# Kernel optimization log

Hardware: AMD Instinct MI355X
Metric: run time of the kernel (lower is better)

## Reference

```python
import jax, jax.numpy as jnp
import numpy as np

N, HIDDEN, HEADS, HEAD = 20000, 128, 8, 16
LAP, NBUCKETS, NBINS, MAXDEG, E = 16, 1024, 32, 64, 320000


def _mlp(x, W1, b1, W2, b2):
    return jax.nn.relu(x @ W1 + b1) @ W2 + b2


def _build_pairs(bq, bk, edge_index):
    """Host-side: P_LSH = {(i,j)!=: bq[i]==bk[j]} union graph edges, deduped.
    Mirrors _lsh_pairs + torch.unique (data-dependent size -> numpy)."""
    bq = np.asarray(bq); bk = np.asarray(bk); ei = np.asarray(edge_index)
    srcs = [ei[0].astype(np.int64)]; dsts = [ei[1].astype(np.int64)]
    common = np.intersect1d(np.unique(bq), np.unique(bk))
    for b in common:
        qn = np.nonzero(bq == b)[0]
        kn = np.nonzero(bk == b)[0]
        ii = np.repeat(qn, kn.size)
        jj = np.tile(kn, qn.size)
        m = ii != jj
        srcs.append(ii[m].astype(np.int64)); dsts.append(jj[m].astype(np.int64))
    src = np.concatenate(srcs); dst = np.concatenate(dsts)
    code = np.unique(src * np.int64(N) + dst)  # dedup pairs
    return jnp.asarray(code // N, jnp.int32), jnp.asarray(code % N, jnp.int32)


def setup_inputs() -> dict:
    key = jax.random.key(0)
    ks = jax.random.split(key, 16)
    rn = lambda k, sh, s=1.0: (jax.random.normal(k, sh, jnp.float32) * s)
    d_in = HIDDEN + LAP
    return {
        "Q": rn(ks[0], (N, HIDDEN)),
        "K": rn(ks[1], (N, HIDDEN)),
        "V": rn(ks[2], (N, HIDDEN)),
        "lap_pe": jax.random.uniform(ks[3], (N, LAP), jnp.float32),
        "W_q1": rn(ks[4], (d_in, HIDDEN), d_in ** -0.5), "b_q1": jnp.zeros((HIDDEN,), jnp.float32),
        "W_q2": rn(ks[5], (HIDDEN, NBUCKETS), HIDDEN ** -0.5), "b_q2": jnp.zeros((NBUCKETS,), jnp.float32),
        "W_k1": rn(ks[6], (d_in, HIDDEN), d_in ** -0.5), "b_k1": jnp.zeros((HIDDEN,), jnp.float32),
        "W_k2": rn(ks[7], (HIDDEN, NBUCKETS), HIDDEN ** -0.5), "b_k2": jnp.zeros((NBUCKETS,), jnp.float32),
        "spd_bias": rn(ks[8], (NBINS + 1, HEADS), 0.02),
        "deg_src_emb": rn(ks[9], (MAXDEG + 2, HEADS), 0.02),
        "deg_dst_emb": rn(ks[10], (MAXDEG + 2, HEADS), 0.02),
        "W_out": rn(ks[11], (HIDDEN, HIDDEN), HIDDEN ** -0.5), "b_out": jnp.zeros((HIDDEN,), jnp.float32),
        "spd_boundaries": jnp.linspace(0.0, 2.0, NBINS).astype(jnp.float32),
        "edge_index": jax.random.randint(ks[12], (2, E), 0, N, jnp.int32),
        "deg": jax.random.randint(ks[13], (N,), 0, MAXDEG + 1, jnp.int32),
    }


def reference(Q, K, V, lap_pe, W_q1, b_q1, W_q2, b_q2, W_k1, b_k1, W_k2, b_k2,
              spd_bias, deg_src_emb, deg_dst_emb, W_out, b_out, spd_boundaries,
              edge_index, deg):
    q_in = jnp.concatenate([Q, lap_pe], axis=-1)
    k_in = jnp.concatenate([K, lap_pe], axis=-1)
    l_q = _mlp(q_in, W_q1, b_q1, W_q2, b_q2)  # (N, B)
    l_k = _mlp(k_in, W_k1, b_k1, W_k2, b_k2)
    src, dst = _build_pairs(jnp.argmax(l_q, -1), jnp.argmax(l_k, -1), edge_index)

    Qh = Q.reshape(N, HEADS, HEAD)
    Kh = K.reshape(N, HEADS, HEAD)
    Vh = V.reshape(N, HEADS, HEAD)

    scores = jnp.einsum("ehd,ehd->eh", Qh[src], Kh[dst]) / (HEAD ** 0.5)  # (P, H)
    pe_dist = jnp.linalg.norm(lap_pe[src] - lap_pe[dst], axis=-1)
    spd_idx = jnp.searchsorted(spd_boundaries, pe_dist, side="left")  # torch.bucketize(right=False)
    scores = scores + spd_bias[spd_idx]
    dsrc = jnp.clip(deg[src], 0, MAXDEG + 1)
    ddst = jnp.clip(deg[dst], 0, MAXDEG + 1)
    scores = scores + deg_src_emb[dsrc] + deg_dst_emb[ddst]

    # pyg_softmax: segment softmax over src index
    m = jax.ops.segment_max(scores, src, num_segments=N)  # (N, H)
    m = jnp.where(jnp.isneginf(m), 0.0, m)
    ex = jnp.exp(scores - m[src])
    denom = jax.ops.segment_sum(ex, src, num_segments=N)
    alpha = ex / (denom[src] + 1e-16)  # dropout p=0 (eval)

    h = jax.ops.segment_sum(alpha[..., None] * Vh[dst], src, num_segments=N)
    h_global = h.reshape(N, HIDDEN) @ W_out + b_out
    return h_global, l_q, l_k
```

## Files before the change

### kernel.cpp

```cpp
#include <hip/hip_runtime.h>
#include <math.h>

#define NN 20000
#define HID 128
#define NH 8
#define HD 16
#define LAPD 16
#define NB 1024
#define NBINS 32
#define MAXDEG 64
#define NE 320000
#define DIN 144

#define NEGH (-1.0e30f)

__global__ __launch_bounds__(256) void mlp_kernel(
    const float* __restrict__ X, const float* __restrict__ lap,
    const float* __restrict__ W1, const float* __restrict__ b1,
    const float* __restrict__ W2, const float* __restrict__ b2,
    float* __restrict__ outL, int* __restrict__ bidx)
{
    __shared__ __align__(16) float xs[16][DIN];
    __shared__ __align__(16) float hs[16][HID];
    __shared__ float rbv[64];
    __shared__ int   rbi[64];
    const int tid = threadIdx.x;
    const int n0 = blockIdx.x * 16;

    for (int e = tid; e < 16 * DIN; e += 256) {
        int n = e / DIN, k = e - n * DIN;
        float v = (k < HID) ? X[(size_t)(n0 + n) * HID + k]
                            : lap[(size_t)(n0 + n) * LAPD + (k - HID)];
        xs[n][k] = v;
    }
    __syncthreads();

    const int c = tid & 127, ng = tid >> 7;
    float hacc[8];
    {
        float bb = b1[c];
        #pragma unroll
        for (int m = 0; m < 8; m++) hacc[m] = bb;
        for (int k = 0; k < DIN; k += 4) {
            float w0 = W1[(k + 0) * HID + c];
            float w1 = W1[(k + 1) * HID + c];
            float w2 = W1[(k + 2) * HID + c];
            float w3 = W1[(k + 3) * HID + c];
            #pragma unroll
            for (int m = 0; m < 8; m++) {
                float4 xv = *(const float4*)&xs[ng * 8 + m][k];
                hacc[m] = fmaf(xv.x, w0, hacc[m]);
                hacc[m] = fmaf(xv.y, w1, hacc[m]);
                hacc[m] = fmaf(xv.z, w2, hacc[m]);
                hacc[m] = fmaf(xv.w, w3, hacc[m]);
            }
        }
    }
    #pragma unroll
    for (int m = 0; m < 8; m++) hs[ng * 8 + m][c] = fmaxf(hacc[m], 0.0f);
    __syncthreads();

    float a0[16], a1[16], a2[16], a3[16];
    #pragma unroll
    for (int m = 0; m < 16; m++) { a0[m] = 0.f; a1[m] = 0.f; a2[m] = 0.f; a3[m] = 0.f; }

    for (int k = 0; k < HID; k += 4) {
        const float4 w0 = *(const float4*)&W2[(size_t)(k + 0) * NB + 4 * tid];
        const float4 w1 = *(const float4*)&W2[(size_t)(k + 1) * NB + 4 * tid];
        const float4 w2 = *(const float4*)&W2[(size_t)(k + 2) * NB + 4 * tid];
        const float4 w3 = *(const float4*)&W2[(size_t)(k + 3) * NB + 4 * tid];
        #pragma unroll
        for (int m = 0; m < 16; m++) {
            const float4 hv = *(const float4*)&hs[m][k];
            a0[m] = fmaf(hv.x, w0.x, fmaf(hv.y, w1.x, fmaf(hv.z, w2.x, fmaf(hv.w, w3.x, a0[m]))));
            a1[m] = fmaf(hv.x, w0.y, fmaf(hv.y, w1.y, fmaf(hv.z, w2.y, fmaf(hv.w, w3.y, a1[m]))));
            a2[m] = fmaf(hv.x, w0.z, fmaf(hv.y, w1.z, fmaf(hv.z, w2.z, fmaf(hv.w, w3.z, a2[m]))));
            a3[m] = fmaf(hv.x, w0.w, fmaf(hv.y, w1.w, fmaf(hv.z, w2.w, fmaf(hv.w, w3.w, a3[m]))));
        }
    }

    const float4 bb4 = *(const float4*)&b2[4 * tid];
    const int lane = tid & 63, wv = tid >> 6;
    const int o0 = 4 * tid;
    for (int m = 0; m < 16; m++) {
        float4 ov;
        ov.x = a0[m] + bb4.x; ov.y = a1[m] + bb4.y;
        ov.z = a2[m] + bb4.z; ov.w = a3[m] + bb4.w;
        *(float4*)&outL[(size_t)(n0 + m) * NB + o0] = ov;
        float bv = ov.x; int bi = o0;
        if (ov.y > bv) { bv = ov.y; bi = o0 + 1; }
        if (ov.z > bv) { bv = ov.z; bi = o0 + 2; }
        if (ov.w > bv) { bv = ov.w; bi = o0 + 3; }
        #pragma unroll
        for (int off = 1; off < 64; off <<= 1) {
            float ovv = __shfl_xor(bv, off, 64);
            int   oi  = __shfl_xor(bi, off, 64);
            if (ovv > bv || (ovv == bv && oi < bi)) { bv = ovv; bi = oi; }
        }
        if (lane == 0) { rbv[wv * 16 + m] = bv; rbi[wv * 16 + m] = bi; }
    }
    __syncthreads();
    if (tid < 16) {
        float bv = rbv[tid]; int bi = rbi[tid];
        #pragma unroll
        for (int ww = 1; ww < 4; ww++) {
            float ov = rbv[ww * 16 + tid]; int oi = rbi[ww * 16 + tid];
            if (ov > bv || (ov == bv && oi < bi)) { bv = ov; bi = oi; }
        }
        bidx[n0 + tid] = min(max(bi, 0), NB - 1);
    }
}

__global__ void zero_kernel(int* __restrict__ p, int n) {
    int i = blockIdx.x * 256 + threadIdx.x;
    if (i < n) p[i] = 0;
}

__global__ void hist_kernel(const int* __restrict__ bkarr, int* __restrict__ bcnt) {
    int i = blockIdx.x * 256 + threadIdx.x;
    if (i < NN) {
        int b = min(max(bkarr[i], 0), NB - 1);
        atomicAdd(&bcnt[b], 1);
    }
}

__global__ __launch_bounds__(1024) void scan_bucket_kernel(const int* __restrict__ cnt,
        int* __restrict__ off, int* __restrict__ fill) {
    __shared__ int s[1024];
    int t = threadIdx.x;
    int v = cnt[t];
    s[t] = v; __syncthreads();
    for (int o = 1; o < 1024; o <<= 1) {
        int a = (t >= o) ? s[t - o] : 0;
        __syncthreads();
        s[t] += a;
        __syncthreads();
    }
    int excl = s[t] - v;
    off[t] = excl; fill[t] = excl;
    if (t == 1023) off[NB] = s[1023];
}

__global__ __launch_bounds__(1024) void scan_edge_kernel(const int* __restrict__ cnt,
        int* __restrict__ off, int* __restrict__ fill) {
    __shared__ int s[1024];
    const int t = threadIdx.x;
    const int base = t * 20;
    int loc[20]; int sum = 0;
    #pragma unroll
    for (int k = 0; k < 20; k++) {
        int idx = base + k;
        int v = (idx < NN) ? cnt[idx] : 0;
        loc[k] = sum; sum += v;
    }
    s[t] = sum; __syncthreads();
    for (int o = 1; o < 1024; o <<= 1) {
        int a = (t >= o) ? s[t - o] : 0;
        __syncthreads();
        s[t] += a;
        __syncthreads();
    }
    int pre = s[t] - sum;
    #pragma unroll
    for (int k = 0; k < 20; k++) {
        int idx = base + k;
        if (idx < NN) { int e = pre + loc[k]; off[idx] = e; fill[idx] = e; }
    }
    if (t == 1023) off[NN] = s[1023];
}

__global__ void scatter_bucket_kernel(const int* __restrict__ bkarr,
        int* __restrict__ fill, int* __restrict__ blist) {
    int i = blockIdx.x * 256 + threadIdx.x;
    if (i < NN) {
        int b = min(max(bkarr[i], 0), NB - 1);
        int p = atomicAdd(&fill[b], 1);
        if (p >= 0 && p < NN) blist[p] = i;
    }
}

__global__ void edge_count_kernel(const int* __restrict__ ei, int* __restrict__ ecnt) {
    int e = blockIdx.x * 256 + threadIdx.x;
    if (e < NE) {
        int s = min(max(ei[e], 0), NN - 1);
        atomicAdd(&ecnt[s], 1);
    }
}

__global__ void edge_scatter_kernel(const int* __restrict__ ei,
        int* __restrict__ fill, int* __restrict__ adj) {
    int e = blockIdx.x * 256 + threadIdx.x;
    if (e < NE) {
        int s = min(max(ei[e], 0), NN - 1);
        int d = min(max(ei[NE + e], 0), NN - 1);
        int p = atomicAdd(&fill[s], 1);
        if (p >= 0 && p < NE) adj[p] = d;
    }
}

__global__ __launch_bounds__(256) void dedup_kernel(
    const int* __restrict__ eoff, int* __restrict__ adj,
    const int* __restrict__ bqv, const int* __restrict__ bkv,
    int* __restrict__ acnt)
{
    __shared__ int prev[4][192];
    const int lane = threadIdx.x & 63, wv = threadIdx.x >> 6;
    const int i = blockIdx.x * 4 + wv;
    if (i >= NN) return;
    int es = eoff[i], ee = eoff[i + 1];
    es = min(max(es, 0), NE); ee = min(max(ee, es), NE);
    const int d = ee - es;
    const int b = min(max(bqv[i], 0), NB - 1);
    int kept = 0;
    for (int t0 = 0; t0 < d; t0 += 64) {
        const int t = t0 + lane;
        const bool in = t < d;
        int j = -1;
        if (in) j = min(max(adj[es + t], 0), NN - 1);
        bool keep = in && ((j == i) || (bkv[j] != b));
        const int nin = min(64, d - t0);
        for (int q2 = 0; q2 < nin; q2++) {
            int jq = __shfl(j, q2, 64);
            if (in && q2 < lane && jq == j) keep = false;
        }
        if (t0 > 0 && in) {
            asm volatile("s_waitcnt lgkmcnt(0)" ::: "memory");
            const int np = min(t0, 192);
            for (int q2 = 0; q2 < np; q2++)
                if (prev[wv][q2] == j) keep = false;
        }
        if (in && t < 192) prev[wv][t] = j;
        unsigned long long km = __ballot(keep);
        int pos = __popcll(km & ((1ull << lane) - 1ull));
        if (keep) adj[es + kept + pos] = j;
        kept += (int)__popcll(km);
    }
    if (lane == 0) acnt[i] = kept;
}

__global__ __launch_bounds__(256, 3) void attn_kernel(
    const float* __restrict__ Q, const float* __restrict__ K, const float* __restrict__ V,
    const float* __restrict__ lap,
    const float* __restrict__ spdb, const float* __restrict__ dse,
    const float* __restrict__ dde, const float* __restrict__ bndr,
    const int* __restrict__ deg,
    const int* __restrict__ bq,
    const int* __restrict__ boff, const int* __restrict__ blist,
    const int* __restrict__ eoff, const int* __restrict__ acnt,
    const int* __restrict__ adj, const int* __restrict__ qlist,
    const float* __restrict__ Wout, const float* __restrict__ bout,
    float* __restrict__ outH)
{
    __shared__ __align__(16) float qfl[4][128];
    __shared__ __align__(16) float pefl[4][16];
    __shared__ __align__(16) float hsm[4][128];
    __shared__ float wts[4][8][66];
    __shared__ int   jls[4][64];
    __shared__ __align__(16) float spdbs[(NBINS + 1) * NH];
    __shared__ __align__(16) float ddes[(MAXDEG + 2) * NH];
    __shared__ float bnd[32];

    const int tid = threadIdx.x;
    const int wv = tid >> 6, lane = tid & 63;
    const int cq = lane >> 2, qq = lane & 3;

    int blk = (int)blockIdx.x;
    blk = (blk & 7) * 625 + (blk >> 3);
    const int task = blk * 4 + wv;
    int i = qlist[task];
    i = min(max(i, 0), NN - 1);

    for (int e = tid; e < (NBINS + 1) * NH; e += 256) spdbs[e] = spdb[e];
    for (int e = tid; e < (MAXDEG + 2) * NH; e += 256) ddes[e] = dde[e];
    if (tid < 32) bnd[tid] = bndr[tid];
    qfl[wv][lane]      = Q[(size_t)i * HID + lane];
    qfl[wv][lane + 64] = Q[(size_t)i * HID + 64 + lane];
    if (lane < 16) pefl[wv][lane] = lap[(size_t)i * LAPD + lane];

    int b = min(max(bq[i], 0), NB - 1);
    int bs = boff[b], be = boff[b + 1];
    bs = min(max(bs, 0), NN); be = min(max(be, bs), NN);
    int es = eoff[i];
    es = min(max(es, 0), NE);
    int na = min(max(acnt[i], 0), NE - es);
    const int Lb = be - bs;
    const int Ltot = Lb + na;
    const int degi = min(max(deg[i], 0), MAXDEG + 1);
    __syncthreads();

    const float4 ds0 = *(const float4*)&dse[degi * 8];
    const float4 ds1 = *(const float4*)&dse[degi * 8 + 4];

    float m8[8], l8[8];
    #pragma unroll
    for (int h = 0; h < 8; h++) { m8[h] = NEGH; l8[h] = 0.0f; }
    float acc[32];
    #pragma unroll
    for (int k = 0; k < 32; k++) acc[k] = 0.0f;

    for (int t0 = 0; t0 < Ltot; t0 += 64) {
        const int t = t0 + lane;
        int j = i; bool valid = false;
        if (t < Ltot) {
            if (t < Lb) {
                j = min(max(blist[bs + t], 0), NN - 1);
                valid = (j != i);
            } else {
                j = min(max(adj[es + (t - Lb)], 0), NN - 1);
                valid = true;
            }
        }

        float s8[8];
        if (valid) {
            const float4* K4 = (const float4*)(K + (size_t)j * HID);
            const float4* Q4 = (const float4*)&qfl[wv][0];
            #pragma unroll
            for (int h = 0; h < 8; h++) {
                float4 k0 = K4[h * 4 + 0], k1 = K4[h * 4 + 1];
                float4 k2 = K4[h * 4 + 2], k3 = K4[h * 4 + 3];
                float4 q0 = Q4[h * 4 + 0], q1 = Q4[h * 4 + 1];
                float4 q2 = Q4[h * 4 + 2], q3 = Q4[h * 4 + 3];
                float dot = 0.0f;
                dot = fmaf(q0.x, k0.x, dot); dot = fmaf(q0.y, k0.y, dot);
                dot = fmaf(q0.z, k0.z, dot); dot = fmaf(q0.w, k0.w, dot);
                dot = fmaf(q1.x, k1.x, dot); dot = fmaf(q1.y, k1.y, dot);
                dot = fmaf(q1.z, k1.z, dot); dot = fmaf(q1.w, k1.w, dot);
                dot = fmaf(q2.x, k2.x, dot); dot = fmaf(q2.y, k2.y, dot);
                dot = fmaf(q2.z, k2.z, dot); dot = fmaf(q2.w, k2.w, dot);
                dot = fmaf(q3.x, k3.x, dot); dot = fmaf(q3.y, k3.y, dot);
                dot = fmaf(q3.z, k3.z, dot); dot = fmaf(q3.w, k3.w, dot);
                s8[h] = dot * 0.25f;
            }
            const float4* P4 = (const float4*)&pefl[wv][0];
            const float4* L4 = (const float4*)(lap + (size_t)j * LAPD);
            float ss = 0.0f;
            #pragma unroll
            for (int d4 = 0; d4 < 4; d4++) {
                float4 pe = P4[d4], lj = L4[d4];
                float dx = pe.x - lj.x, dy = pe.y - lj.y;
                float dz = pe.z - lj.z, dw = pe.w - lj.w;
                ss = fmaf(dx, dx, ss); ss = fmaf(dy, dy, ss);
                ss = fmaf(dz, dz, ss); ss = fmaf(dw, dw, ss);
            }
            float dist = sqrtf(ss);
            int si = 0;
            #pragma unroll
            for (int kb = 0; kb < 32; kb++) si += (bnd[kb] < dist) ? 1 : 0;
            const int dj = min(max(deg[j], 0), MAXDEG + 1);
            const float4 sb0 = *(const float4*)&spdbs[si * 8];
            const float4 sb1 = *(const float4*)&spdbs[si * 8 + 4];
            const float4 db0 = *(const float4*)&ddes[dj * 8];
            const float4 db1 = *(const float4*)&ddes[dj * 8 + 4];
            s8[0] += sb0.x + ds0.x + db0.x; s8[1] += sb0.y + ds0.y + db0.y;
            s8[2] += sb0.z + ds0.z + db0.z; s8[3] += sb0.w + ds0.w + db0.w;
            s8[4] += sb1.x + ds1.x + db1.x; s8[5] += sb1.y + ds1.y + db1.y;
            s8[6] += sb1.z + ds1.z + db1.z; s8[7] += sb1.w + ds1.w + db1.w;
        } else {
            #pragma unroll
            for (int h = 0; h < 8; h++) s8[h] = NEGH;
        }

        float alpha8[8];
        #pragma unroll
        for (int h = 0; h < 8; h++) {
            float cm = s8[h];
            #pragma unroll
            for (int off = 1; off < 64; off <<= 1)
                cm = fmaxf(cm, __shfl_xor(cm, off, 64));
            const float mn = fmaxf(m8[h], cm);
            alpha8[h] = __expf(m8[h] - mn);
            const float p = valid ? __expf(s8[h] - mn) : 0.0f;
            l8[h] = l8[h] * alpha8[h] + p;
            m8[h] = mn;
            wts[wv][h][lane] = p;
        }
        jls[wv][lane] = valid ? j : i;

        float aq0, aq1;
        if (qq == 0)      { aq0 = alpha8[0]; aq1 = alpha8[1]; }
        else if (qq == 1) { aq0 = alpha8[2]; aq1 = alpha8[3]; }
        else if (qq == 2) { aq0 = alpha8[4]; aq1 = alpha8[5]; }
        else              { aq0 = alpha8[6]; aq1 = alpha8[7]; }

        #pragma unroll
        for (int k = 0; k < 16; k++) acc[k] *= aq0;
        #pragma unroll
        for (int k = 16; k < 32; k++) acc[k] *= aq1;

        asm volatile("s_waitcnt lgkmcnt(0)" ::: "memory");

        const int rem = Ltot - t0;
        const int npass = ((rem < 64 ? rem : 64) + 15) >> 4;
        for (int r = 0; r < npass; r++) {
            const int cc = r * 16 + cq;
            const int jc = jls[wv][cc];
            const float w0 = wts[wv][2 * qq][cc];
            const float w1 = wts[wv][2 * qq + 1][cc];
            const float4* V4 = (const float4*)(V + (size_t)jc * HID + qq * 32);
            #pragma unroll
            for (int s = 0; s < 4; s++) {
                const float4 v = V4[s];
                acc[s * 4 + 0] = fmaf(w0, v.x, acc[s * 4 + 0]);
                acc[s * 4 + 1] = fmaf(w0, v.y, acc[s * 4 + 1]);
                acc[s * 4 + 2] = fmaf(w0, v.z, acc[s * 4 + 2]);
                acc[s * 4 + 3] = fmaf(w0, v.w, acc[s * 4 + 3]);
            }
            #pragma unroll
            for (int s = 4; s < 8; s++) {
                const float4 v = V4[s];
                acc[s * 4 + 0] = fmaf(w1, v.x, acc[s * 4 + 0]);
                acc[s * 4 + 1] = fmaf(w1, v.y, acc[s * 4 + 1]);
                acc[s * 4 + 2] = fmaf(w1, v.z, acc[s * 4 + 2]);
                acc[s * 4 + 3] = fmaf(w1, v.w, acc[s * 4 + 3]);
            }
        }
    }

    #pragma unroll
    for (int h = 0; h < 8; h++) {
        float v = l8[h];
        #pragma unroll
        for (int off = 1; off < 64; off <<= 1) v += __shfl_xor(v, off, 64);
        l8[h] = v;
    }
    float lq0, lq1;
    if (qq == 0)      { lq0 = l8[0]; lq1 = l8[1]; }
    else if (qq == 1) { lq0 = l8[2]; lq1 = l8[3]; }
    else if (qq == 2) { lq0 = l8[4]; lq1 = l8[5]; }
    else              { lq0 = l8[6]; lq1 = l8[7]; }
    const float linv0 = 1.0f / (lq0 + 1e-16f);
    const float linv1 = 1.0f / (lq1 + 1e-16f);
    #pragma unroll
    for (int k = 0; k < 16; k++) acc[k] *= linv0;
    #pragma unroll
    for (int k = 16; k < 32; k++) acc[k] *= linv1;

    #pragma unroll
    for (int k = 0; k < 32; k++) {
        float v = acc[k];
        v += __shfl_xor(v, 4, 64);
        v += __shfl_xor(v, 8, 64);
        v += __shfl_xor(v, 16, 64);
        v += __shfl_xor(v, 32, 64);
        acc[k] = v;
    }
    if (cq == 0) {
        #pragma unroll
        for (int k = 0; k < 32; k++) hsm[wv][qq * 32 + k] = acc[k];
    }
    asm volatile("s_waitcnt lgkmcnt(0)" ::: "memory");

    float o0 = bout[lane];
    float o1 = bout[lane + 64];
    for (int k = 0; k < HID; k++) {
        const float hk = hsm[wv][k];
        o0 = fmaf(hk, Wout[k * HID + lane], o0);
        o1 = fmaf(hk, Wout[k * HID + 64 + lane], o1);
    }
    outH[(size_t)i * HID + lane]      = o0;
    outH[(size_t)i * HID + 64 + lane] = o1;
}

extern "C" void kernel_launch(void* const* d_in, const int* in_sizes, int n_in,
                              void* d_out, int out_size, void* d_ws, size_t ws_size,
                              hipStream_t stream) {
    const float* Q    = (const float*)d_in[0];
    const float* Kx   = (const float*)d_in[1];
    const float* Vx   = (const float*)d_in[2];
    const float* lap  = (const float*)d_in[3];
    const float* Wq1  = (const float*)d_in[4];
    const float* bq1  = (const float*)d_in[5];
    const float* Wq2  = (const float*)d_in[6];
    const float* bq2  = (const float*)d_in[7];
    const float* Wk1  = (const float*)d_in[8];
    const float* bk1  = (const float*)d_in[9];
    const float* Wk2  = (const float*)d_in[10];
    const float* bk2  = (const float*)d_in[11];
    const float* spdb = (const float*)d_in[12];
    const float* dse  = (const float*)d_in[13];
    const float* dde  = (const float*)d_in[14];
    const float* Wout = (const float*)d_in[15];
    const float* bout = (const float*)d_in[16];
    const float* bndr = (const float*)d_in[17];
    const int*   ei   = (const int*)d_in[18];
    const int*   deg  = (const int*)d_in[19];

    float* out   = (float*)d_out;
    float* outH  = out;
    float* outLq = out + (size_t)NN * HID;
    float* outLk = outLq + (size_t)NN * NB;

    int* wsp = (int*)d_ws;
    size_t o = 0;
    auto carve = [&](size_t n_ints) -> int* {
        int* p = wsp + o; o += n_ints; return p;
    };
    int* bcnt  = carve(NB);
    int* boff  = carve(NB + 1);
    int* bfill = carve(NB);
    int* blist = carve(NN);
    int* bqv   = carve(NN);
    int* bkv   = carve(NN);
    int* ecnt  = carve(NN);
    int* eoff  = carve(NN + 1);
    int* efill = carve(NN);
    int* adj   = carve(NE);
    int* qoff  = carve(NB + 1);
    int* qlist = carve(NN);

    zero_kernel<<<(NB + 255) / 256, 256, 0, stream>>>(bcnt, NB);
    zero_kernel<<<(NN + 255) / 256, 256, 0, stream>>>(ecnt, NN);

    mlp_kernel<<<NN / 16, 256, 0, stream>>>(Q,  lap, Wq1, bq1, Wq2, bq2, outLq, bqv);
    mlp_kernel<<<NN / 16, 256, 0, stream>>>(Kx, lap, Wk1, bk1, Wk2, bk2, outLk, bkv);

    hist_kernel<<<(NN + 255) / 256, 256, 0, stream>>>(bkv, bcnt);
    scan_bucket_kernel<<<1, 1024, 0, stream>>>(bcnt, boff, bfill);
    scatter_bucket_kernel<<<(NN + 255) / 256, 256, 0, stream>>>(bkv, bfill, blist);

    zero_kernel<<<(NB + 255) / 256, 256, 0, stream>>>(bcnt, NB);
    hist_kernel<<<(NN + 255) / 256, 256, 0, stream>>>(bqv, bcnt);
    scan_bucket_kernel<<<1, 1024, 0, stream>>>(bcnt, qoff, bfill);
    scatter_bucket_kernel<<<(NN + 255) / 256, 256, 0, stream>>>(bqv, bfill, qlist);

    edge_count_kernel<<<(NE + 255) / 256, 256, 0, stream>>>(ei, ecnt);
    scan_edge_kernel<<<1, 1024, 0, stream>>>(ecnt, eoff, efill);
    edge_scatter_kernel<<<(NE + 255) / 256, 256, 0, stream>>>(ei, efill, adj);

    dedup_kernel<<<NN / 4, 256, 0, stream>>>(eoff, adj, bqv, bkv, ecnt);

    attn_kernel<<<NN / 4, 256, 0, stream>>>(Q, Kx, Vx, lap, spdb, dse, dde, bndr, deg,
                                            bqv, boff, blist, eoff, ecnt, adj, qlist,
                                            Wout, bout, outH);
}
```

Measured before the change: 882.6 us.

## Split output projection into tiled GEMM kernel and prefetch neighbor indices and weights

The per-node Wout projection moves out of the attention kernel into a separate tiled GEMM kernel that reuses each Wout load across 16 rows. The attention kernel now writes raw h into outH, which the new kernel reads back in place. Neighbor indices for the next 64-wide chunk are prefetched during the current chunk, and the MLP's W2 loads are software-pipelined one k-step ahead. The launch_bounds occupancy hint on attn_kernel is dropped, which may raise register use and lower occupancy, and the extra launch adds a global round-trip of h.

After: 845.3 us. 4.2% less time.

```diff
diff --git a/kernel.cpp b/kernel.cpp
--- a/kernel.cpp
+++ b/kernel.cpp
@@ -64,11 +64,17 @@
     #pragma unroll
     for (int m = 0; m < 16; m++) { a0[m] = 0.f; a1[m] = 0.f; a2[m] = 0.f; a3[m] = 0.f; }
 
+    const float* W2b = W2 + 4 * tid;
+    float4 w0 = *(const float4*)&W2b[(size_t)0 * NB];
+    float4 w1 = *(const float4*)&W2b[(size_t)1 * NB];
+    float4 w2 = *(const float4*)&W2b[(size_t)2 * NB];
+    float4 w3 = *(const float4*)&W2b[(size_t)3 * NB];
     for (int k = 0; k < HID; k += 4) {
-        const float4 w0 = *(const float4*)&W2[(size_t)(k + 0) * NB + 4 * tid];
-        const float4 w1 = *(const float4*)&W2[(size_t)(k + 1) * NB + 4 * tid];
-        const float4 w2 = *(const float4*)&W2[(size_t)(k + 2) * NB + 4 * tid];
-        const float4 w3 = *(const float4*)&W2[(size_t)(k + 3) * NB + 4 * tid];
+        const int kn = (k + 4 < HID) ? (k + 4) : 0;
+        float4 nw0 = *(const float4*)&W2b[(size_t)(kn + 0) * NB];
+        float4 nw1 = *(const float4*)&W2b[(size_t)(kn + 1) * NB];
+        float4 nw2 = *(const float4*)&W2b[(size_t)(kn + 2) * NB];
+        float4 nw3 = *(const float4*)&W2b[(size_t)(kn + 3) * NB];
         #pragma unroll
         for (int m = 0; m < 16; m++) {
             const float4 hv = *(const float4*)&hs[m][k];
@@ -77,6 +83,7 @@
             a2[m] = fmaf(hv.x, w0.z, fmaf(hv.y, w1.z, fmaf(hv.z, w2.z, fmaf(hv.w, w3.z, a2[m]))));
             a3[m] = fmaf(hv.x, w0.w, fmaf(hv.y, w1.w, fmaf(hv.z, w2.w, fmaf(hv.w, w3.w, a3[m]))));
         }
+        w0 = nw0; w1 = nw1; w2 = nw2; w3 = nw3;
     }
 
     const float4 bb4 = *(const float4*)&b2[4 * tid];
@@ -238,7 +245,7 @@
     if (lane == 0) acnt[i] = kept;
 }
 
-__global__ __launch_bounds__(256, 3) void attn_kernel(
+__global__ __launch_bounds__(256) void attn_kernel(
     const float* __restrict__ Q, const float* __restrict__ K, const float* __restrict__ V,
     const float* __restrict__ lap,
     const float* __restrict__ spdb, const float* __restrict__ dse,
@@ -248,12 +255,10 @@
     const int* __restrict__ boff, const int* __restrict__ blist,
     const int* __restrict__ eoff, const int* __restrict__ acnt,
     const int* __restrict__ adj, const int* __restrict__ qlist,
-    const float* __restrict__ Wout, const float* __restrict__ bout,
     float* __restrict__ outH)
 {
     __shared__ __align__(16) float qfl[4][128];
     __shared__ __align__(16) float pefl[4][16];
-    __shared__ __align__(16) float hsm[4][128];
     __shared__ float wts[4][8][66];
     __shared__ int   jls[4][64];
     __shared__ __align__(16) float spdbs[(NBINS + 1) * NH];
@@ -286,6 +291,17 @@
     const int Lb = be - bs;
     const int Ltot = Lb + na;
     const int degi = min(max(deg[i], 0), MAXDEG + 1);
+
+    int jn = i; bool vn = false;
+    if (lane < Ltot) {
+        if (lane < Lb) {
+            jn = min(max(blist[bs + lane], 0), NN - 1);
+            vn = (jn != i);
+        } else {
+            jn = min(max(adj[es + (lane - Lb)], 0), NN - 1);
+            vn = true;
+        }
+    }
     __syncthreads();
 
     const float4 ds0 = *(const float4*)&dse[degi * 8];
@@ -299,17 +315,7 @@
     for (int k = 0; k < 32; k++) acc[k] = 0.0f;
 
     for (int t0 = 0; t0 < Ltot; t0 += 64) {
-        const int t = t0 + lane;
-        int j = i; bool valid = false;
-        if (t < Ltot) {
-            if (t < Lb) {
-                j = min(max(blist[bs + t], 0), NN - 1);
-                valid = (j != i);
-            } else {
-                j = min(max(adj[es + (t - Lb)], 0), NN - 1);
-                valid = true;
-            }
-        }
+        const int j = jn; const bool valid = vn;
 
         float s8[8];
         if (valid) {
@@ -360,6 +366,21 @@
             #pragma unroll
             for (int h = 0; h < 8; h++) s8[h] = NEGH;
         }
+        jls[wv][lane] = valid ? j : i;
+
+        jn = i; vn = false;
+        {
+            const int t2 = t0 + 64 + lane;
+            if (t2 < Ltot) {
+                if (t2 < Lb) {
+                    jn = min(max(blist[bs + t2], 0), NN - 1);
+                    vn = (jn != i);
+                } else {
+                    jn = min(max(adj[es + (t2 - Lb)], 0), NN - 1);
+                    vn = true;
+                }
+            }
+        }
 
         float alpha8[8];
         #pragma unroll
@@ -375,7 +396,6 @@
             m8[h] = mn;
             wts[wv][h][lane] = p;
         }
-        jls[wv][lane] = valid ? j : i;
 
         float aq0, aq1;
         if (qq == 0)      { aq0 = alpha8[0]; aq1 = alpha8[1]; }
@@ -446,20 +466,49 @@
         acc[k] = v;
     }
     if (cq == 0) {
-        #pragma unroll
-        for (int k = 0; k < 32; k++) hsm[wv][qq * 32 + k] = acc[k];
-    }
-    asm volatile("s_waitcnt lgkmcnt(0)" ::: "memory");
-
-    float o0 = bout[lane];
-    float o1 = bout[lane + 64];
-    for (int k = 0; k < HID; k++) {
-        const float hk = hsm[wv][k];
-        o0 = fmaf(hk, Wout[k * HID + lane], o0);
-        o1 = fmaf(hk, Wout[k * HID + 64 + lane], o1);
-    }
-    outH[(size_t)i * HID + lane]      = o0;
-    outH[(size_t)i * HID + 64 + lane] = o1;
+        float4* orow = (float4*)(outH + (size_t)i * HID + qq * 32);
+        #pragma unroll
+        for (int s = 0; s < 8; s++)
+            orow[s] = make_float4(acc[s * 4 + 0], acc[s * 4 + 1],
+                                  acc[s * 4 + 2], acc[s * 4 + 3]);
+    }
+}
+
+__global__ __launch_bounds__(256) void out_gemm_kernel(
+    const float* __restrict__ Wout, const float* __restrict__ bout,
+    float* __restrict__ outH)
+{
+    __shared__ __align__(16) float hsT[32][HID];
+    const int tid = threadIdx.x;
+    const int r0 = blockIdx.x * 32;
+
+    for (int e = tid; e < 32 * 32; e += 256) {
+        const int r = e >> 5, c4 = e & 31;
+        ((float4*)&hsT[r][0])[c4] = ((const float4*)&outH[(size_t)(r0 + r) * HID])[c4];
+    }
+    __syncthreads();
+
+    const int c = tid & 127;
+    const int mg = tid >> 7;
+    float acc[16];
+    const float bb = bout[c];
+    #pragma unroll
+    for (int m = 0; m < 16; m++) acc[m] = bb;
+
+    for (int k = 0; k < HID; k += 4) {
+        const float w0 = Wout[(size_t)(k + 0) * HID + c];
+        const float w1 = Wout[(size_t)(k + 1) * HID + c];
+        const float w2 = Wout[(size_t)(k + 2) * HID + c];
+        const float w3 = Wout[(size_t)(k + 3) * HID + c];
+        #pragma unroll
+        for (int m = 0; m < 16; m++) {
+            const float4 hv = *(const float4*)&hsT[mg * 16 + m][k];
+            acc[m] = fmaf(hv.x, w0, fmaf(hv.y, w1, fmaf(hv.z, w2, fmaf(hv.w, w3, acc[m]))));
+        }
+    }
+    #pragma unroll
+    for (int m = 0; m < 16; m++)
+        outH[(size_t)(r0 + mg * 16 + m) * HID + c] = acc[m];
 }
 
 extern "C" void kernel_launch(void* const* d_in, const int* in_sizes, int n_in,
@@ -532,5 +581,7 @@
 
     attn_kernel<<<NN / 4, 256, 0, stream>>>(Q, Kx, Vx, lap, spdb, dse, dde, bndr, deg,
                                             bqv, boff, blist, eoff, ecnt, adj, qlist,
-                                            Wout, bout, outH);
-}
+                                            outH);
+
+    out_gemm_kernel<<<NN / 32, 256, 0, stream>>>(Wout, bout, outH);
+}
```
